# Kernel tuning notes

Measured on AMD Instinct MI355X. Metric: run time of the kernel, lower is better.

The kernel has to match this reference:

```python
import jax, jax.numpy as jnp
import numpy as np

EMBED_DIM = 768
NUM_HEADS = 12
HEAD_DIM = EMBED_DIM // NUM_HEADS


def setup_inputs() -> dict:
    key = jax.random.key(0)
    k_x, k_wqkv, k_bqkv, k_wo, k_bo = jax.random.split(key, 5)
    B, S, D = 4, 2048, EMBED_DIM
    bound = 1.0 / np.sqrt(D)
    x = jax.random.normal(k_x, (B, S, D), dtype=jnp.float32)
    # nn.Linear weights: torch stores [out, in]; we keep same layout and use x @ W.T
    W_qkv = jax.random.uniform(k_wqkv, (3 * D, D), jnp.float32, -bound, bound)
    b_qkv = jax.random.uniform(k_bqkv, (3 * D,), jnp.float32, -bound, bound)
    W_out = jax.random.uniform(k_wo, (D, D), jnp.float32, -bound, bound)
    b_out = jax.random.uniform(k_bo, (D,), jnp.float32, -bound, bound)
    return {"x": x, "W_qkv": W_qkv, "b_qkv": b_qkv, "W_out": W_out, "b_out": b_out}


def reference(x, W_qkv, b_qkv, W_out, b_out):
    B, S, D = x.shape
    H, Hd = NUM_HEADS, HEAD_DIM
    qkv = x @ W_qkv.T + b_qkv                       # [B,S,3D]
    qkv = qkv.reshape(B, S, H, 3 * Hd).transpose(0, 2, 1, 3)  # [B,H,S,3Hd]
    q, k, v = jnp.split(qkv, 3, axis=-1)            # each [B,H,S,Hd]
    scale = Hd ** -0.5
    scores = jnp.einsum("bhsd,bhtd->bhst", q, k) * scale  # [B,H,S,S]
    weights = jax.nn.softmax(scores, axis=-1)
    ctx = jnp.einsum("bhst,bhtd->bhsd", weights, v)       # [B,H,S,Hd]
    ctx = ctx.transpose(0, 2, 1, 3).reshape(B, S, D)      # [B,S,D]
    return ctx @ W_out.T + b_out
```

## Files before the change

kernel.cpp:

```cpp
#include <hip/hip_runtime.h>
#include <hip/hip_bf16.h>
#include <stdint.h>
#include <math.h>

typedef unsigned short u16;
typedef __attribute__((ext_vector_type(8))) short short8;
typedef __attribute__((ext_vector_type(4))) short short4v;
typedef __attribute__((ext_vector_type(4))) float f32x4;
typedef __attribute__((ext_vector_type(16))) float f32x16;
typedef __attribute__((ext_vector_type(4))) unsigned int u32x4;
typedef __attribute__((ext_vector_type(2))) unsigned int u32x2;

#define NB 4
#define NS 2048
#define NH 12
#define HD 64
#define ND 768
#define ND3 2304

#define QSCALE 0.18033688f

__device__ __forceinline__ u16 f2bf(float f) {
    unsigned int u = __float_as_uint(f);
    unsigned int r = u + 0x7fffu + ((u >> 16) & 1u);
    return (u16)(r >> 16);
}

__device__ __forceinline__ void gload16(const u16* g, u16* s) {
    __builtin_amdgcn_global_load_lds(
        (const __attribute__((address_space(1))) unsigned int*)(const void*)g,
        (__attribute__((address_space(3))) unsigned int*)(void*)s, 16, 0, 0);
}

#define XN4   1572864
#define WQN4  442368
#define WON4  147456
__global__ __launch_bounds__(256) void castall(const float* __restrict__ x,
                                               const float* __restrict__ wq,
                                               const float* __restrict__ wo,
                                               u16* __restrict__ xb,
                                               u16* __restrict__ wqb,
                                               u16* __restrict__ wob) {
    int i = blockIdx.x * 256 + threadIdx.x;
    const float* s; u16* d; int j;
    if (i < XN4) { s = x; d = xb; j = i; }
    else if (i < XN4 + WQN4) { s = wq; d = wqb; j = i - XN4; }
    else if (i < XN4 + WQN4 + WON4) { s = wo; d = wob; j = i - XN4 - WQN4; }
    else return;
    float4 v = ((const float4*)s)[j];
    ushort4 o;
    o.x = f2bf(v.x); o.y = f2bf(v.y); o.z = f2bf(v.z); o.w = f2bf(v.w);
    ((ushort4*)d)[j] = o;
}

__global__ __launch_bounds__(256, 3) void gemm_qkv(const u16* __restrict__ A,
                                                   const u16* __restrict__ Bw,
                                                   const float* __restrict__ bias,
                                                   u16* __restrict__ Qg,
                                                   u16* __restrict__ Kg,
                                                   u16* __restrict__ Vtg) {
    __shared__ u16 lds[2][10240];
    const int tid = threadIdx.x;
    const int w = tid >> 6, l = tid & 63;
    const int lam = l & 15, quad = l >> 4;
    const int wm = w >> 1, wn = w & 1;
    const int bm = blockIdx.x * 128;
    const int hh = blockIdx.y;
    const int bn = hh * 192;
    const int K = ND;

    f32x4 acc[4][6];
#pragma unroll
    for (int i = 0; i < 4; i++)
#pragma unroll
        for (int j = 0; j < 6; j++) { f32x4 z = {0.f, 0.f, 0.f, 0.f}; acc[i][j] = z; }

    const u16* gp[5];
    int so[5];
#pragma unroll
    for (int i = 0; i < 5; i++) {
        int c = w * 5 + i;
        if (c < 8) { gp[i] = A + (size_t)(bm + c * 16 + lam) * K + quad * 8; so[i] = c * 512; }
        else { int nf = c - 8; gp[i] = Bw + (size_t)(bn + nf * 16 + lam) * K + quad * 8; so[i] = 4096 + nf * 512; }
    }

#pragma unroll
    for (int i = 0; i < 5; i++) gload16(gp[i], &lds[0][so[i]]);
    asm volatile("s_waitcnt vmcnt(0)" ::: "memory");
    __syncthreads();

    int cur = 0;
    for (int k0 = 0; k0 < K; k0 += 32) {
        if (k0 + 32 < K) {
#pragma unroll
            for (int i = 0; i < 5; i++) gload16(gp[i] + k0 + 32, &lds[cur ^ 1][so[i]]);
        }
        short8 a[4];
#pragma unroll
        for (int i = 0; i < 4; i++) a[i] = *(const short8*)(&lds[cur][(wm * 4 + i) * 512 + l * 8]);
#pragma unroll
        for (int half = 0; half < 2; half++) {
            short8 b[3];
#pragma unroll
            for (int j = 0; j < 3; j++) b[j] = *(const short8*)(&lds[cur][4096 + (wn * 6 + half * 3 + j) * 512 + l * 8]);
#pragma unroll
            for (int mf = 0; mf < 4; mf++)
#pragma unroll
                for (int j = 0; j < 3; j++)
                    acc[mf][half * 3 + j] = __builtin_amdgcn_mfma_f32_16x16x32_bf16(a[mf], b[j], acc[mf][half * 3 + j], 0, 0, 0);
        }
        asm volatile("s_waitcnt vmcnt(0)" ::: "memory");
        __syncthreads();
        cur ^= 1;
    }

#pragma unroll
    for (int nf = 0; nf < 6; nf++) {
        int nloc = wn * 96 + nf * 16;
        int rgn = nloc / 64;
        int d = (nloc % 64) + lam;
        float bv = bias[bn + nloc + lam];
        if (rgn == 2) {
#pragma unroll
            for (int mf = 0; mf < 4; mf++) {
                int m0 = bm + wm * 64 + mf * 16 + quad * 4;
                int bq = m0 >> 11, s0 = m0 & 2047;
                ushort4 o;
                o.x = f2bf(acc[mf][nf][0] + bv);
                o.y = f2bf(acc[mf][nf][1] + bv);
                o.z = f2bf(acc[mf][nf][2] + bv);
                o.w = f2bf(acc[mf][nf][3] + bv);
                *(ushort4*)(Vtg + ((size_t)((bq * NH + hh) * HD + d)) * NS + s0) = o;
            }
        } else {
            u16* dst = (rgn == 0) ? Qg : Kg;
            const float sc = (rgn == 0) ? QSCALE : 1.0f;
#pragma unroll
            for (int mf = 0; mf < 4; mf++)
#pragma unroll
                for (int r = 0; r < 4; r++) {
                    int m = bm + wm * 64 + mf * 16 + quad * 4 + r;
                    int bq = m >> 11, s = m & 2047;
                    dst[((size_t)((bq * NH + hh) * NS + s)) * HD + d] = f2bf((acc[mf][nf][r] + bv) * sc);
                }
        }
    }
}

__global__ __launch_bounds__(256, 3) void attn(const u16* __restrict__ Qg,
                                               const u16* __restrict__ Kg,
                                               const u16* __restrict__ Vtg,
                                               u16* __restrict__ ctx) {
    __shared__ u16 kt_lds[8192];
    __shared__ u16 vt_lds[8192];
    const int tid = threadIdx.x;
    const int w = tid >> 6, L = tid & 63;
    const int r5 = L & 31, h = L >> 5;
    const int bid = blockIdx.x;
    const int qt = bid / 48, bh = bid % 48;
    const int b = bh / NH, hd = bh % NH;
    const u16* Qh = Qg + (size_t)bh * NS * HD;
    const u16* Kh = Kg + (size_t)bh * NS * HD;
    const u16* Vh = Vtg + (size_t)bh * HD * NS;

    const int qbase = qt * 128 + w * 32;

    short8 qf[4];
#pragma unroll
    for (int s = 0; s < 4; s++)
        qf[s] = *(const short8*)(Qh + (size_t)(qbase + r5) * HD + s * 16 + h * 8);

    f32x16 ot[2];
#pragma unroll
    for (int hg = 0; hg < 2; hg++)
#pragma unroll
        for (int r = 0; r < 16; r++) ot[hg][r] = 0.f;

    f32x16 lsum;
#pragma unroll
    for (int r = 0; r < 16; r++) lsum[r] = 0.f;
    short8 onesf;
#pragma unroll
    for (int i = 0; i < 8; i++) onesf[i] = (short)0x3F80;

    f32x16 zero16;
#pragma unroll
    for (int r = 0; r < 16; r++) zero16[r] = 0.f;
    asm volatile("" : "+v"(zero16));

    const u16* gp[8];
    u16* sp[8];
    int step;
    if (w < 2) {
#pragma unroll
        for (int i = 0; i < 8; i++) {
            int c = w * 8 + i, kg = c >> 2, s = c & 3;
            gp[i] = Kh + (size_t)(kg * 32 + r5) * HD + s * 16 + h * 8;
            sp[i] = kt_lds + c * 512;
        }
        step = 128 * HD;
    } else {
#pragma unroll
        for (int i = 0; i < 8; i++) {
            int c = (w - 2) * 8 + i;
            gp[i] = Vh + (size_t)((c >> 3) * 32 + r5) * NS + (c & 7) * 16 + h * 8;
            sp[i] = vt_lds + c * 512;
        }
        step = 128;
    }

    u32x4 rg[8];
#pragma unroll
    for (int i = 0; i < 8; i++) { rg[i] = *(const u32x4*)gp[i]; gp[i] += step; }

    for (int kt = 0; kt < 16; kt++) {
        __syncthreads();
#pragma unroll
        for (int i = 0; i < 8; i++) *(u32x4*)(sp[i] + (size_t)L * 8) = rg[i];
        __syncthreads();

        if (kt < 15) {
#pragma unroll
            for (int i = 0; i < 8; i++) { rg[i] = *(const u32x4*)gp[i]; gp[i] += step; }
        }

#pragma unroll
        for (int kg = 0; kg < 4; kg++) {
            __builtin_amdgcn_s_setprio(1);
            short8 kf0 = *(const short8*)(kt_lds + (kg * 4 + 0) * 512 + L * 8);
            f32x16 st = __builtin_amdgcn_mfma_f32_32x32x16_bf16(kf0, qf[0], zero16, 0, 0, 0);
#pragma unroll
            for (int s = 1; s < 4; s++) {
                short8 kf = *(const short8*)(kt_lds + (kg * 4 + s) * 512 + L * 8);
                st = __builtin_amdgcn_mfma_f32_32x32x16_bf16(kf, qf[s], st, 0, 0, 0);
            }
            __builtin_amdgcn_s_setprio(0);

            float e[16];
#pragma unroll
            for (int i = 0; i < 16; i++) e[i] = __builtin_amdgcn_exp2f(st[i]);
            unsigned int q8[8];
#pragma unroll
            for (int i = 0; i < 8; i++) {
                unsigned int pk;
                asm("v_cvt_pk_bf16_f32 %0, %1, %2" : "=v"(pk) : "v"(e[2 * i]), "v"(e[2 * i + 1]));
                q8[i] = pk;
            }
            u32x2 s02 = __builtin_amdgcn_permlane32_swap(q8[0], q8[2], false, false);
            u32x2 s13 = __builtin_amdgcn_permlane32_swap(q8[1], q8[3], false, false);
            u32x2 s46 = __builtin_amdgcn_permlane32_swap(q8[4], q8[6], false, false);
            u32x2 s57 = __builtin_amdgcn_permlane32_swap(q8[5], q8[7], false, false);
            union { u32x4 u; short8 s; } af0, af1;
            af0.u = (u32x4){s02.x, s13.x, s02.y, s13.y};
            af1.u = (u32x4){s46.x, s57.x, s46.y, s57.y};

            __builtin_amdgcn_s_setprio(1);
            lsum = __builtin_amdgcn_mfma_f32_32x32x16_bf16(af0.s, onesf, lsum, 0, 0, 0);
            lsum = __builtin_amdgcn_mfma_f32_32x32x16_bf16(af1.s, onesf, lsum, 0, 0, 0);
#pragma unroll
            for (int hg = 0; hg < 2; hg++) {
                short8 vf0 = *(const short8*)(vt_lds + (hg * 8 + kg * 2 + 0) * 512 + L * 8);
                short8 vf1 = *(const short8*)(vt_lds + (hg * 8 + kg * 2 + 1) * 512 + L * 8);
                ot[hg] = __builtin_amdgcn_mfma_f32_32x32x16_bf16(af0.s, vf0, ot[hg], 0, 0, 0);
                ot[hg] = __builtin_amdgcn_mfma_f32_32x32x16_bf16(af1.s, vf1, ot[hg], 0, 0, 0);
            }
            __builtin_amdgcn_s_setprio(0);
        }
    }

    float inv[16];
#pragma unroll
    for (int r = 0; r < 16; r++) inv[r] = __builtin_amdgcn_rcpf(lsum[r]);
#pragma unroll
    for (int hg = 0; hg < 2; hg++) {
#pragma unroll
        for (int r = 0; r < 16; r++) {
            int q = qbase + (r & 3) + 8 * (r >> 2) + 4 * h;
            ctx[(size_t)(b * NS + q) * ND + hd * HD + hg * 32 + r5] = f2bf(ot[hg][r] * inv[r]);
        }
    }
}

__global__ __launch_bounds__(256) void gemm_out(const u16* __restrict__ A,
                                                const u16* __restrict__ Bw,
                                                const float* __restrict__ bias,
                                                float* __restrict__ out) {
    __shared__ u16 lds[2][7168];
    const int tid = threadIdx.x;
    const int w = tid >> 6, l = tid & 63;
    const int lam = l & 15, quad = l >> 4;
    const int wm = w >> 1, wn = w & 1;
    const int bm = blockIdx.x * 128, bn = blockIdx.y * 96;
    const int K = ND;

    f32x4 acc[4][3];
#pragma unroll
    for (int i = 0; i < 4; i++)
#pragma unroll
        for (int j = 0; j < 3; j++) { f32x4 z = {0.f, 0.f, 0.f, 0.f}; acc[i][j] = z; }

    const u16* gp[4];
    int so[4];
#pragma unroll
    for (int i = 0; i < 4; i++) {
        int c = w * 4 + i;
        if (c >= 14) c -= 14;
        if (c < 8) { gp[i] = A + (size_t)(bm + c * 16 + lam) * K + quad * 8; so[i] = c * 512; }
        else { int nf = c - 8; gp[i] = Bw + (size_t)(bn + nf * 16 + lam) * K + quad * 8; so[i] = 4096 + nf * 512; }
    }

#pragma unroll
    for (int i = 0; i < 4; i++) gload16(gp[i], &lds[0][so[i]]);
    asm volatile("s_waitcnt vmcnt(0)" ::: "memory");
    __syncthreads();

    int cur = 0;
    for (int k0 = 0; k0 < K; k0 += 32) {
        if (k0 + 32 < K) {
#pragma unroll
            for (int i = 0; i < 4; i++) gload16(gp[i] + k0 + 32, &lds[cur ^ 1][so[i]]);
        }
        short8 a[4], b[3];
#pragma unroll
        for (int i = 0; i < 4; i++) a[i] = *(const short8*)(&lds[cur][(wm * 4 + i) * 512 + l * 8]);
#pragma unroll
        for (int j = 0; j < 3; j++) b[j] = *(const short8*)(&lds[cur][4096 + (wn * 3 + j) * 512 + l * 8]);
#pragma unroll
        for (int mf = 0; mf < 4; mf++)
#pragma unroll
            for (int j = 0; j < 3; j++)
                acc[mf][j] = __builtin_amdgcn_mfma_f32_16x16x32_bf16(a[mf], b[j], acc[mf][j], 0, 0, 0);
        asm volatile("s_waitcnt vmcnt(0)" ::: "memory");
        __syncthreads();
        cur ^= 1;
    }

#pragma unroll
    for (int nf = 0; nf < 3; nf++) {
        int n = bn + wn * 48 + nf * 16 + lam;
        float bv = bias[n];
#pragma unroll
        for (int mf = 0; mf < 4; mf++)
#pragma unroll
            for (int r = 0; r < 4; r++) {
                int m = bm + wm * 64 + mf * 16 + quad * 4 + r;
                out[(size_t)m * ND + n] = acc[mf][nf][r] + bv;
            }
    }
}

extern "C" void kernel_launch(void* const* d_in, const int* in_sizes, int n_in,
                              void* d_out, int out_size, void* d_ws, size_t ws_size,
                              hipStream_t stream) {
    const float* x    = (const float*)d_in[0];
    const float* Wqkv = (const float*)d_in[1];
    const float* bqkv = (const float*)d_in[2];
    const float* Wout = (const float*)d_in[3];
    const float* bout = (const float*)d_in[4];
    float* out = (float*)d_out;

    u16* p = (u16*)d_ws;
    u16* xb    = p; p += 6291456;
    u16* wqkvb = p; p += 1769472;
    u16* wob   = p; p += 589824;
    u16* Qg    = p; p += 6291456;
    u16* Kg    = p; p += 6291456;
    u16* Vtg   = p; p += 6291456;
    u16* ctx   = p; p += 6291456;

    castall<<<8448, 256, 0, stream>>>(x, Wqkv, Wout, xb, wqkvb, wob);
    gemm_qkv<<<dim3(64, 12), 256, 0, stream>>>(xb, wqkvb, bqkv, Qg, Kg, Vtg);
    attn<<<768, 256, 0, stream>>>(Qg, Kg, Vtg, ctx);
    gemm_out<<<dim3(64, 8), 256, 0, stream>>>(ctx, wob, bout, out);
}
```

Before: 224.5 us.

## Fuse fp32-to-bf16 cast of x into QKV GEMM load path; drop attn setprio

The cast kernel no longer converts the activation tensor x. The QKV GEMM now reads fp32 x directly into registers, converts to bf16 with packed cvt instructions and writes the A tile to LDS, while B still uses direct global-to-LDS loads. This removes a full write and re-read of a bf16 copy of x, but each of the 12 column blocks now re-reads fp32 x, doubling A-side traffic per block, and register pressure rises. The s_setprio hints around the MFMA sections in the attention kernel are also removed.

```diff
diff --git a/kernel.cpp b/kernel.cpp
--- a/kernel.cpp
+++ b/kernel.cpp
@@ -32,20 +32,22 @@
         (__attribute__((address_space(3))) unsigned int*)(void*)s, 16, 0, 0);
 }
 
-#define XN4   1572864
+__device__ __forceinline__ unsigned int cvtpk(float lo, float hi) {
+    unsigned int pk;
+    asm("v_cvt_pk_bf16_f32 %0, %1, %2" : "=v"(pk) : "v"(lo), "v"(hi));
+    return pk;
+}
+
 #define WQN4  442368
 #define WON4  147456
-__global__ __launch_bounds__(256) void castall(const float* __restrict__ x,
-                                               const float* __restrict__ wq,
-                                               const float* __restrict__ wo,
-                                               u16* __restrict__ xb,
-                                               u16* __restrict__ wqb,
-                                               u16* __restrict__ wob) {
+__global__ __launch_bounds__(256) void castw(const float* __restrict__ wq,
+                                             const float* __restrict__ wo,
+                                             u16* __restrict__ wqb,
+                                             u16* __restrict__ wob) {
     int i = blockIdx.x * 256 + threadIdx.x;
     const float* s; u16* d; int j;
-    if (i < XN4) { s = x; d = xb; j = i; }
-    else if (i < XN4 + WQN4) { s = wq; d = wqb; j = i - XN4; }
-    else if (i < XN4 + WQN4 + WON4) { s = wo; d = wob; j = i - XN4 - WQN4; }
+    if (i < WQN4) { s = wq; d = wqb; j = i; }
+    else if (i < WQN4 + WON4) { s = wo; d = wob; j = i - WQN4; }
     else return;
     float4 v = ((const float4*)s)[j];
     ushort4 o;
@@ -53,7 +55,7 @@
     ((ushort4*)d)[j] = o;
 }
 
-__global__ __launch_bounds__(256, 3) void gemm_qkv(const u16* __restrict__ A,
+__global__ __launch_bounds__(256, 3) void gemm_qkv(const float* __restrict__ X,
                                                    const u16* __restrict__ Bw,
                                                    const float* __restrict__ bias,
                                                    u16* __restrict__ Qg,
@@ -75,25 +77,49 @@
 #pragma unroll
         for (int j = 0; j < 6; j++) { f32x4 z = {0.f, 0.f, 0.f, 0.f}; acc[i][j] = z; }
 
-    const u16* gp[5];
-    int so[5];
-#pragma unroll
-    for (int i = 0; i < 5; i++) {
-        int c = w * 5 + i;
-        if (c < 8) { gp[i] = A + (size_t)(bm + c * 16 + lam) * K + quad * 8; so[i] = c * 512; }
-        else { int nf = c - 8; gp[i] = Bw + (size_t)(bn + nf * 16 + lam) * K + quad * 8; so[i] = 4096 + nf * 512; }
-    }
-
-#pragma unroll
-    for (int i = 0; i < 5; i++) gload16(gp[i], &lds[0][so[i]]);
-    asm volatile("s_waitcnt vmcnt(0)" ::: "memory");
-    __syncthreads();
+    const float* ga[2]; int soA[2];
+#pragma unroll
+    for (int i = 0; i < 2; i++) {
+        int c = w * 2 + i;
+        ga[i] = X + (size_t)(bm + c * 16 + lam) * K + quad * 8;
+        soA[i] = c * 512;
+    }
+    const u16* gb[3]; int soB[3];
+#pragma unroll
+    for (int j = 0; j < 3; j++) {
+        int nf = w * 3 + j;
+        gb[j] = Bw + (size_t)(bn + nf * 16 + lam) * K + quad * 8;
+        soB[j] = 4096 + nf * 512;
+    }
+
+    {
+        float4 f0[2], f1[2];
+#pragma unroll
+        for (int i = 0; i < 2; i++) { f0[i] = *(const float4*)(ga[i]); f1[i] = *(const float4*)(ga[i] + 4); }
+#pragma unroll
+        for (int j = 0; j < 3; j++) gload16(gb[j], &lds[0][soB[j]]);
+#pragma unroll
+        for (int i = 0; i < 2; i++) {
+            u32x4 pk;
+            pk.x = cvtpk(f0[i].x, f0[i].y); pk.y = cvtpk(f0[i].z, f0[i].w);
+            pk.z = cvtpk(f1[i].x, f1[i].y); pk.w = cvtpk(f1[i].z, f1[i].w);
+            *(u32x4*)(&lds[0][soA[i] + l * 8]) = pk;
+        }
+        asm volatile("s_waitcnt vmcnt(0)" ::: "memory");
+        __syncthreads();
+    }
 
     int cur = 0;
     for (int k0 = 0; k0 < K; k0 += 32) {
+        float4 f0[2], f1[2];
         if (k0 + 32 < K) {
 #pragma unroll
-            for (int i = 0; i < 5; i++) gload16(gp[i] + k0 + 32, &lds[cur ^ 1][so[i]]);
+            for (int i = 0; i < 2; i++) {
+                f0[i] = *(const float4*)(ga[i] + k0 + 32);
+                f1[i] = *(const float4*)(ga[i] + k0 + 36);
+            }
+#pragma unroll
+            for (int j = 0; j < 3; j++) gload16(gb[j] + k0 + 32, &lds[cur ^ 1][soB[j]]);
         }
         short8 a[4];
 #pragma unroll
@@ -108,6 +134,15 @@
 #pragma unroll
                 for (int j = 0; j < 3; j++)
                     acc[mf][half * 3 + j] = __builtin_amdgcn_mfma_f32_16x16x32_bf16(a[mf], b[j], acc[mf][half * 3 + j], 0, 0, 0);
+        }
+        if (k0 + 32 < K) {
+#pragma unroll
+            for (int i = 0; i < 2; i++) {
+                u32x4 pk;
+                pk.x = cvtpk(f0[i].x, f0[i].y); pk.y = cvtpk(f0[i].z, f0[i].w);
+                pk.z = cvtpk(f1[i].x, f1[i].y); pk.w = cvtpk(f1[i].z, f1[i].w);
+                *(u32x4*)(&lds[cur ^ 1][soA[i] + l * 8]) = pk;
+            }
         }
         asm volatile("s_waitcnt vmcnt(0)" ::: "memory");
         __syncthreads();
@@ -226,7 +261,6 @@
 
 #pragma unroll
         for (int kg = 0; kg < 4; kg++) {
-            __builtin_amdgcn_s_setprio(1);
             short8 kf0 = *(const short8*)(kt_lds + (kg * 4 + 0) * 512 + L * 8);
             f32x16 st = __builtin_amdgcn_mfma_f32_32x32x16_bf16(kf0, qf[0], zero16, 0, 0, 0);
 #pragma unroll
@@ -234,18 +268,14 @@
                 short8 kf = *(const short8*)(kt_lds + (kg * 4 + s) * 512 + L * 8);
                 st = __builtin_amdgcn_mfma_f32_32x32x16_bf16(kf, qf[s], st, 0, 0, 0);
             }
-            __builtin_amdgcn_s_setprio(0);
 
             float e[16];
 #pragma unroll
             for (int i = 0; i < 16; i++) e[i] = __builtin_amdgcn_exp2f(st[i]);
             unsigned int q8[8];
 #pragma unroll
-            for (int i = 0; i < 8; i++) {
-                unsigned int pk;
-                asm("v_cvt_pk_bf16_f32 %0, %1, %2" : "=v"(pk) : "v"(e[2 * i]), "v"(e[2 * i + 1]));
-                q8[i] = pk;
-            }
+            for (int i = 0; i < 8; i++) q8[i] = cvtpk(e[2 * i], e[2 * i + 1]);
+
             u32x2 s02 = __builtin_amdgcn_permlane32_swap(q8[0], q8[2], false, false);
             u32x2 s13 = __builtin_amdgcn_permlane32_swap(q8[1], q8[3], false, false);
             u32x2 s46 = __builtin_amdgcn_permlane32_swap(q8[4], q8[6], false, false);
@@ -254,7 +284,6 @@
             af0.u = (u32x4){s02.x, s13.x, s02.y, s13.y};
             af1.u = (u32x4){s46.x, s57.x, s46.y, s57.y};
 
-            __builtin_amdgcn_s_setprio(1);
             lsum = __builtin_amdgcn_mfma_f32_32x32x16_bf16(af0.s, onesf, lsum, 0, 0, 0);
             lsum = __builtin_amdgcn_mfma_f32_32x32x16_bf16(af1.s, onesf, lsum, 0, 0, 0);
 #pragma unroll
@@ -264,7 +293,6 @@
                 ot[hg] = __builtin_amdgcn_mfma_f32_32x32x16_bf16(af0.s, vf0, ot[hg], 0, 0, 0);
                 ot[hg] = __builtin_amdgcn_mfma_f32_32x32x16_bf16(af1.s, vf1, ot[hg], 0, 0, 0);
             }
-            __builtin_amdgcn_s_setprio(0);
         }
     }
 
@@ -360,7 +388,6 @@
     float* out = (float*)d_out;
 
     u16* p = (u16*)d_ws;
-    u16* xb    = p; p += 6291456;
     u16* wqkvb = p; p += 1769472;
     u16* wob   = p; p += 589824;
     u16* Qg    = p; p += 6291456;
@@ -368,8 +395,8 @@
     u16* Vtg   = p; p += 6291456;
     u16* ctx   = p; p += 6291456;
 
-    castall<<<8448, 256, 0, stream>>>(x, Wqkv, Wout, xb, wqkvb, wob);
-    gemm_qkv<<<dim3(64, 12), 256, 0, stream>>>(xb, wqkvb, bqkv, Qg, Kg, Vtg);
+    castw<<<2304, 256, 0, stream>>>(Wqkv, Wout, wqkvb, wob);
+    gemm_qkv<<<dim3(64, 12), 256, 0, stream>>>(x, wqkvb, bqkv, Qg, Kg, Vtg);
     attn<<<768, 256, 0, stream>>>(Qg, Kg, Vtg, ctx);
     gemm_out<<<dim3(64, 8), 256, 0, stream>>>(ctx, wob, bout, out);
 }
```

Measured after the change: 241.4 us. 7.5% more time.

## Deepen GEMM LDS pipelines to four stages with partial vmcnt waits

Applied to the files above, without the earlier changes.

Both projection GEMMs switch from a double-buffered LDS loop that waited for all loads each iteration to a four-buffer ring that prefetches three K-tiles ahead. Each iteration waits with a counted vmcnt, so later loads stay in flight while earlier tiles are consumed, and only one barrier is used per step. The goal is to hide global-load latency better, at the cost of doubling LDS use, which lowers occupancy (launch bounds now target 2 blocks per CU). The attention kernel also drops its s_setprio hints and factors the bf16 pack into a helper.

```diff
diff --git a/kernel.cpp b/kernel.cpp
--- a/kernel.cpp
+++ b/kernel.cpp
@@ -5,7 +5,6 @@
 
 typedef unsigned short u16;
 typedef __attribute__((ext_vector_type(8))) short short8;
-typedef __attribute__((ext_vector_type(4))) short short4v;
 typedef __attribute__((ext_vector_type(4))) float f32x4;
 typedef __attribute__((ext_vector_type(16))) float f32x16;
 typedef __attribute__((ext_vector_type(4))) unsigned int u32x4;
@@ -30,6 +29,12 @@
     __builtin_amdgcn_global_load_lds(
         (const __attribute__((address_space(1))) unsigned int*)(const void*)g,
         (__attribute__((address_space(3))) unsigned int*)(void*)s, 16, 0, 0);
+}
+
+__device__ __forceinline__ unsigned int cvtpk(float lo, float hi) {
+    unsigned int pk;
+    asm("v_cvt_pk_bf16_f32 %0, %1, %2" : "=v"(pk) : "v"(lo), "v"(hi));
+    return pk;
 }
 
 #define XN4   1572864
@@ -53,13 +58,13 @@
     ((ushort4*)d)[j] = o;
 }
 
-__global__ __launch_bounds__(256, 3) void gemm_qkv(const u16* __restrict__ A,
+__global__ __launch_bounds__(256, 2) void gemm_qkv(const u16* __restrict__ A,
                                                    const u16* __restrict__ Bw,
                                                    const float* __restrict__ bias,
                                                    u16* __restrict__ Qg,
                                                    u16* __restrict__ Kg,
                                                    u16* __restrict__ Vtg) {
-    __shared__ u16 lds[2][10240];
+    __shared__ u16 lds[4][10240];
     const int tid = threadIdx.x;
     const int w = tid >> 6, l = tid & 63;
     const int lam = l & 15, quad = l >> 4;
@@ -67,7 +72,7 @@
     const int bm = blockIdx.x * 128;
     const int hh = blockIdx.y;
     const int bn = hh * 192;
-    const int K = ND;
+    const int NT = ND / 32;
 
     f32x4 acc[4][6];
 #pragma unroll
@@ -80,38 +85,40 @@
 #pragma unroll
     for (int i = 0; i < 5; i++) {
         int c = w * 5 + i;
-        if (c < 8) { gp[i] = A + (size_t)(bm + c * 16 + lam) * K + quad * 8; so[i] = c * 512; }
-        else { int nf = c - 8; gp[i] = Bw + (size_t)(bn + nf * 16 + lam) * K + quad * 8; so[i] = 4096 + nf * 512; }
-    }
-
-#pragma unroll
-    for (int i = 0; i < 5; i++) gload16(gp[i], &lds[0][so[i]]);
-    asm volatile("s_waitcnt vmcnt(0)" ::: "memory");
-    __syncthreads();
-
-    int cur = 0;
-    for (int k0 = 0; k0 < K; k0 += 32) {
-        if (k0 + 32 < K) {
-#pragma unroll
-            for (int i = 0; i < 5; i++) gload16(gp[i] + k0 + 32, &lds[cur ^ 1][so[i]]);
-        }
+        if (c < 8) { gp[i] = A + (size_t)(bm + c * 16 + lam) * ND + quad * 8; so[i] = c * 512; }
+        else { int nf = c - 8; gp[i] = Bw + (size_t)(bn + nf * 16 + lam) * ND + quad * 8; so[i] = 4096 + nf * 512; }
+    }
+
+#pragma unroll
+    for (int t = 0; t < 3; t++)
+#pragma unroll
+        for (int i = 0; i < 5; i++) gload16(gp[i] + t * 32, &lds[t][so[i]]);
+
+    for (int t = 0; t < NT; ++t) {
+        if (t < NT - 2)      asm volatile("s_waitcnt vmcnt(10)" ::: "memory");
+        else if (t == NT - 2) asm volatile("s_waitcnt vmcnt(5)" ::: "memory");
+        else                 asm volatile("s_waitcnt vmcnt(0)" ::: "memory");
+        __builtin_amdgcn_s_barrier();
+        asm volatile("" ::: "memory");
+        if (t + 3 < NT) {
+#pragma unroll
+            for (int i = 0; i < 5; i++) gload16(gp[i] + (t + 3) * 32, &lds[(t + 3) & 3][so[i]]);
+        }
+        const u16* buf = lds[t & 3];
         short8 a[4];
 #pragma unroll
-        for (int i = 0; i < 4; i++) a[i] = *(const short8*)(&lds[cur][(wm * 4 + i) * 512 + l * 8]);
+        for (int i = 0; i < 4; i++) a[i] = *(const short8*)(buf + (wm * 4 + i) * 512 + l * 8);
 #pragma unroll
         for (int half = 0; half < 2; half++) {
             short8 b[3];
 #pragma unroll
-            for (int j = 0; j < 3; j++) b[j] = *(const short8*)(&lds[cur][4096 + (wn * 6 + half * 3 + j) * 512 + l * 8]);
+            for (int j = 0; j < 3; j++) b[j] = *(const short8*)(buf + 4096 + (wn * 6 + half * 3 + j) * 512 + l * 8);
 #pragma unroll
             for (int mf = 0; mf < 4; mf++)
 #pragma unroll
                 for (int j = 0; j < 3; j++)
                     acc[mf][half * 3 + j] = __builtin_amdgcn_mfma_f32_16x16x32_bf16(a[mf], b[j], acc[mf][half * 3 + j], 0, 0, 0);
         }
-        asm volatile("s_waitcnt vmcnt(0)" ::: "memory");
-        __syncthreads();
-        cur ^= 1;
     }
 
 #pragma unroll
@@ -226,7 +233,6 @@
 
 #pragma unroll
         for (int kg = 0; kg < 4; kg++) {
-            __builtin_amdgcn_s_setprio(1);
             short8 kf0 = *(const short8*)(kt_lds + (kg * 4 + 0) * 512 + L * 8);
             f32x16 st = __builtin_amdgcn_mfma_f32_32x32x16_bf16(kf0, qf[0], zero16, 0, 0, 0);
 #pragma unroll
@@ -234,18 +240,14 @@
                 short8 kf = *(const short8*)(kt_lds + (kg * 4 + s) * 512 + L * 8);
                 st = __builtin_amdgcn_mfma_f32_32x32x16_bf16(kf, qf[s], st, 0, 0, 0);
             }
-            __builtin_amdgcn_s_setprio(0);
 
             float e[16];
 #pragma unroll
             for (int i = 0; i < 16; i++) e[i] = __builtin_amdgcn_exp2f(st[i]);
             unsigned int q8[8];
 #pragma unroll
-            for (int i = 0; i < 8; i++) {
-                unsigned int pk;
-                asm("v_cvt_pk_bf16_f32 %0, %1, %2" : "=v"(pk) : "v"(e[2 * i]), "v"(e[2 * i + 1]));
-                q8[i] = pk;
-            }
+            for (int i = 0; i < 8; i++) q8[i] = cvtpk(e[2 * i], e[2 * i + 1]);
+
             u32x2 s02 = __builtin_amdgcn_permlane32_swap(q8[0], q8[2], false, false);
             u32x2 s13 = __builtin_amdgcn_permlane32_swap(q8[1], q8[3], false, false);
             u32x2 s46 = __builtin_amdgcn_permlane32_swap(q8[4], q8[6], false, false);
@@ -254,7 +256,6 @@
             af0.u = (u32x4){s02.x, s13.x, s02.y, s13.y};
             af1.u = (u32x4){s46.x, s57.x, s46.y, s57.y};
 
-            __builtin_amdgcn_s_setprio(1);
             lsum = __builtin_amdgcn_mfma_f32_32x32x16_bf16(af0.s, onesf, lsum, 0, 0, 0);
             lsum = __builtin_amdgcn_mfma_f32_32x32x16_bf16(af1.s, onesf, lsum, 0, 0, 0);
 #pragma unroll
@@ -264,7 +265,6 @@
                 ot[hg] = __builtin_amdgcn_mfma_f32_32x32x16_bf16(af0.s, vf0, ot[hg], 0, 0, 0);
                 ot[hg] = __builtin_amdgcn_mfma_f32_32x32x16_bf16(af1.s, vf1, ot[hg], 0, 0, 0);
             }
-            __builtin_amdgcn_s_setprio(0);
         }
     }
 
@@ -281,17 +281,17 @@
     }
 }
 
-__global__ __launch_bounds__(256) void gemm_out(const u16* __restrict__ A,
-                                                const u16* __restrict__ Bw,
-                                                const float* __restrict__ bias,
-                                                float* __restrict__ out) {
-    __shared__ u16 lds[2][7168];
+__global__ __launch_bounds__(256, 2) void gemm_out(const u16* __restrict__ A,
+                                                   const u16* __restrict__ Bw,
+                                                   const float* __restrict__ bias,
+                                                   float* __restrict__ out) {
+    __shared__ u16 lds[4][7168];
     const int tid = threadIdx.x;
     const int w = tid >> 6, l = tid & 63;
     const int lam = l & 15, quad = l >> 4;
     const int wm = w >> 1, wn = w & 1;
     const int bm = blockIdx.x * 128, bn = blockIdx.y * 96;
-    const int K = ND;
+    const int NT = ND / 32;
 
     f32x4 acc[4][3];
 #pragma unroll
@@ -305,34 +305,36 @@
     for (int i = 0; i < 4; i++) {
         int c = w * 4 + i;
         if (c >= 14) c -= 14;
-        if (c < 8) { gp[i] = A + (size_t)(bm + c * 16 + lam) * K + quad * 8; so[i] = c * 512; }
-        else { int nf = c - 8; gp[i] = Bw + (size_t)(bn + nf * 16 + lam) * K + quad * 8; so[i] = 4096 + nf * 512; }
-    }
-
-#pragma unroll
-    for (int i = 0; i < 4; i++) gload16(gp[i], &lds[0][so[i]]);
-    asm volatile("s_waitcnt vmcnt(0)" ::: "memory");
-    __syncthreads();
-
-    int cur = 0;
-    for (int k0 = 0; k0 < K; k0 += 32) {
-        if (k0 + 32 < K) {
-#pragma unroll
-            for (int i = 0; i < 4; i++) gload16(gp[i] + k0 + 32, &lds[cur ^ 1][so[i]]);
-        }
+        if (c < 8) { gp[i] = A + (size_t)(bm + c * 16 + lam) * ND + quad * 8; so[i] = c * 512; }
+        else { int nf = c - 8; gp[i] = Bw + (size_t)(bn + nf * 16 + lam) * ND + quad * 8; so[i] = 4096 + nf * 512; }
+    }
+
+#pragma unroll
+    for (int t = 0; t < 3; t++)
+#pragma unroll
+        for (int i = 0; i < 4; i++) gload16(gp[i] + t * 32, &lds[t][so[i]]);
+
+    for (int t = 0; t < NT; ++t) {
+        if (t < NT - 2)      asm volatile("s_waitcnt vmcnt(8)" ::: "memory");
+        else if (t == NT - 2) asm volatile("s_waitcnt vmcnt(4)" ::: "memory");
+        else                 asm volatile("s_waitcnt vmcnt(0)" ::: "memory");
+        __builtin_amdgcn_s_barrier();
+        asm volatile("" ::: "memory");
+        if (t + 3 < NT) {
+#pragma unroll
+            for (int i = 0; i < 4; i++) gload16(gp[i] + (t + 3) * 32, &lds[(t + 3) & 3][so[i]]);
+        }
+        const u16* buf = lds[t & 3];
         short8 a[4], b[3];
 #pragma unroll
-        for (int i = 0; i < 4; i++) a[i] = *(const short8*)(&lds[cur][(wm * 4 + i) * 512 + l * 8]);
-#pragma unroll
-        for (int j = 0; j < 3; j++) b[j] = *(const short8*)(&lds[cur][4096 + (wn * 3 + j) * 512 + l * 8]);
+        for (int i = 0; i < 4; i++) a[i] = *(const short8*)(buf + (wm * 4 + i) * 512 + l * 8);
+#pragma unroll
+        for (int j = 0; j < 3; j++) b[j] = *(const short8*)(buf + 4096 + (wn * 3 + j) * 512 + l * 8);
 #pragma unroll
         for (int mf = 0; mf < 4; mf++)
 #pragma unroll
             for (int j = 0; j < 3; j++)
                 acc[mf][j] = __builtin_amdgcn_mfma_f32_16x16x32_bf16(a[mf], b[j], acc[mf][j], 0, 0, 0);
-        asm volatile("s_waitcnt vmcnt(0)" ::: "memory");
-        __syncthreads();
-        cur ^= 1;
     }
 
 #pragma unroll
```

Result: no change. 222.5 us (-0.9%).
